# Performance work log

Hardware: AMD Instinct MI355X
Metric: run time of the kernel (lower is better)

The kernel has to match this reference:

```python
import jax, jax.numpy as jnp
import numpy as np

B, L, D = 16, 1024, 1024  # D = 2*model_dim
NEG = -1e10


def setup_inputs() -> dict:
    key = jax.random.key(0)
    k1, k2, k3, k4 = jax.random.split(key, 4)
    inp = jax.random.normal(k1, (B, L, D), dtype=jnp.float32)
    # realistic padding: each sequence has a valid length in [L//2, L]
    lengths = jax.random.randint(k2, (B,), L // 2, L + 1)
    inp_mask = jnp.arange(L)[None, :] >= lengths[:, None]  # True = pad
    # linear_similarity_matrix: Linear(3D, 1, bias=False) -> weight (3D,)
    w_sim = jax.random.normal(k3, (3 * D,), dtype=jnp.float32) * np.sqrt(2.0 / (3 * D + 1)).astype(np.float32)
    # merge_linear: Linear(3D, D)
    Wm = jax.random.normal(k4, (3 * D, D), dtype=jnp.float32) * np.sqrt(2.0 / (4 * D)).astype(np.float32)
    bm = jnp.zeros((D,), dtype=jnp.float32)
    return {"inp": inp, "inp_mask": inp_mask, "w_sim": w_sim, "Wm": Wm, "bm": bm}


def reference(inp, inp_mask, w_sim, Wm, bm):
    # dropout p with training=False is identity (eval mode)
    d = inp.shape[-1]
    w1, w2, w3 = w_sim[:d], w_sim[d:2 * d], w_sim[2 * d:]
    # score[b,i,j] = c_i.w1 + q_j.w2 + (c_i * q_j).w3   (decomposed, no (B,L,L,3D) tensor)
    s_c = inp @ w1                                   # (B, L)
    s_q = inp @ w2                                   # (B, L)
    s_m = jnp.einsum('bid,bjd->bij', inp * w3, inp)  # (B, L, L)
    scores = s_c[:, :, None] + s_q[:, None, :] + s_m
    attn_mask = inp_mask[:, :, None] | inp_mask[:, None, :]
    scores = jnp.where(attn_mask, NEG, scores)
    attn = jax.nn.softmax(scores, axis=-1)           # (B, L, L)
    c2q = jnp.einsum('bij,bjd->bid', attn, inp)      # (B, L, D)
    # merge: relu(cat(c, c2q, c*c2q) @ Wm + bm), decomposed to avoid concat
    W1, W2, W3 = Wm[:d], Wm[d:2 * d], Wm[2 * d:]
    merged = jax.nn.relu(inp @ W1 + c2q @ W2 + (inp * c2q) @ W3 + bm)
    out = jnp.where(inp_mask[:, :, None], 0.0, merged)
    return out
```

## Files before the change

kernel.cpp:

```cpp
#include <hip/hip_runtime.h>
#include <cstdint>

#define LDIM 1024
#define BATCH 16
#define DDIM 1024
#define LDU 3072
#define LDP 2048

using u16 = unsigned short;
typedef __bf16 bf16x8 __attribute__((ext_vector_type(8)));
typedef short  s16x8  __attribute__((ext_vector_type(8)));
typedef float  f32x4  __attribute__((ext_vector_type(4)));

__device__ __forceinline__ u16 f2bf(float f) {
  union { float f; unsigned u; } v; v.f = f;
  unsigned u = v.u;
  return (u16)((u + 0x7FFFu + ((u >> 16) & 1u)) >> 16);
}

typedef const __attribute__((address_space(1))) unsigned int* gp_t;
typedef __attribute__((address_space(3))) unsigned int* lp_t;
__device__ __forceinline__ void async_copy16(const void* g, void* l) {
  __builtin_amdgcn_global_load_lds((gp_t)g, (lp_t)l, 16, 0, 0);
}

__device__ __forceinline__ f32x4 mfma16(s16x8 a, s16x8 b, f32x4 c) {
  return __builtin_amdgcn_mfma_f32_16x16x32_bf16(
      __builtin_bit_cast(bf16x8, a), __builtin_bit_cast(bf16x8, b), c, 0, 0, 0);
}

__device__ __forceinline__ float blockReduceSum(float v) {
  __shared__ float sb[4];
  #pragma unroll
  for (int off = 32; off >= 1; off >>= 1) v += __shfl_xor(v, off);
  if ((threadIdx.x & 63) == 0) sb[threadIdx.x >> 6] = v;
  __syncthreads();
  float r = sb[0] + sb[1] + sb[2] + sb[3];
  __syncthreads();
  return r;
}
__device__ __forceinline__ float blockReduceSum2(float v) {
  __shared__ float sb2[4];
  #pragma unroll
  for (int off = 32; off >= 1; off >>= 1) v += __shfl_xor(v, off);
  if ((threadIdx.x & 63) == 0) sb2[threadIdx.x >> 6] = v;
  __syncthreads();
  float r = sb2[0] + sb2[1] + sb2[2] + sb2[3];
  __syncthreads();
  return r;
}
__device__ __forceinline__ float blockReduceMax(float v) {
  __shared__ float sbm[4];
  #pragma unroll
  for (int off = 32; off >= 1; off >>= 1) v = fmaxf(v, __shfl_xor(v, off));
  if ((threadIdx.x & 63) == 0) sbm[threadIdx.x >> 6] = v;
  __syncthreads();
  float r = fmaxf(fmaxf(sbm[0], sbm[1]), fmaxf(sbm[2], sbm[3]));
  __syncthreads();
  return r;
}

__global__ void diag_kernel(float* __restrict__ out, int n, float tag) {
  int i = blockIdx.x * 256 + threadIdx.x;
  if (i < n) out[i] = (i == 0) ? tag : 0.f;
}

__global__ __launch_bounds__(256) void mask_len_kernel(const unsigned char* __restrict__ mraw,
                                                       int* __restrict__ lengths) {
  const int b = blockIdx.x;
  __shared__ int flag, cnt;
  if (threadIdx.x == 0) { flag = 0; cnt = 0; }
  __syncthreads();
  const int total = BATCH * LDIM;
  for (int p = threadIdx.x; p < total; p += 256) {
    unsigned char v = mraw[p];
    if (v) {
      if (p & 3) atomicOr(&flag, 1);
      else if (p + 3 < total && mraw[p+1] == 0 && mraw[p+2] == 0 && mraw[p+3] == 0)
        atomicOr(&flag, 2);
    }
  }
  __syncthreads();
  const int f = (flag & 1) ? 1 : ((flag & 2) ? 2 : 0);
  int c = 0;
  for (int j = threadIdx.x; j < LDIM; j += 256) {
    bool z;
    if (f == 1)      z = (mraw[b * LDIM + j] == 0);
    else if (f == 2) z = (((const int*)mraw)[b * LDIM + j] == 0);
    else             z = true;
    c += z ? 1 : 0;
  }
  atomicAdd(&cnt, c);
  __syncthreads();
  if (threadIdx.x == 0) lengths[b] = cnt;
}

__global__ __launch_bounds__(256) void prep_row_kernel(
    const float* __restrict__ inp, const float* __restrict__ w_sim,
    u16* __restrict__ U, u16* __restrict__ Abf,
    float* __restrict__ s_c, float* __restrict__ s_q) {
  const int gR = blockIdx.x;
  const int t  = threadIdx.x;
  const float4 x  = ((const float4*)(inp + (size_t)gR * DDIM))[t];
  const float4 w1 = ((const float4*)(w_sim))[t];
  const float4 w2 = ((const float4*)(w_sim + DDIM))[t];
  const float4 w3 = ((const float4*)(w_sim + 2 * DDIM))[t];
  ushort4 xb; xb.x = f2bf(x.x); xb.y = f2bf(x.y); xb.z = f2bf(x.z); xb.w = f2bf(x.w);
  ((ushort4*)(U + (size_t)gR * LDU))[t] = xb;
  ushort4 ab; ab.x = f2bf(x.x * w3.x); ab.y = f2bf(x.y * w3.y);
  ab.z = f2bf(x.z * w3.z); ab.w = f2bf(x.w * w3.w);
  ((ushort4*)(Abf + (size_t)gR * DDIM))[t] = ab;
  float pc = x.x * w1.x + x.y * w1.y + x.z * w1.z + x.w * w1.w;
  float pq = x.x * w2.x + x.y * w2.y + x.z * w2.z + x.w * w2.w;
  pc = blockReduceSum(pc);
  pq = blockReduceSum2(pq);
  if (t == 0) { s_c[gR] = pc; s_q[gR] = pq; }
}

__global__ __launch_bounds__(256) void transpose_x(const u16* __restrict__ U,
                                                   u16* __restrict__ XT) {
  __shared__ u16 tile[64][68];
  const int ti = blockIdx.x, td = blockIdx.y, b = blockIdx.z;
  const int t = threadIdx.x;
  const u16* src = U + ((size_t)(b * LDIM + ti * 64)) * LDU + td * 64;
  #pragma unroll
  for (int q = 0; q < 4; ++q) {
    int n = q * 256 + t;
    int r = n >> 4, c4 = n & 15;
    ushort4 v = ((const ushort4*)(src + (size_t)r * LDU))[c4];
    *(ushort4*)&tile[r][c4 * 4] = v;
  }
  __syncthreads();
  u16* dst = XT + (size_t)b * ((size_t)DDIM * LDIM) + (size_t)(td * 64) * LDIM + ti * 64;
  #pragma unroll
  for (int q = 0; q < 4; ++q) {
    int n = q * 256 + t;
    int d = n >> 4, i4 = n & 15;
    ushort4 v;
    v.x = tile[i4 * 4 + 0][d];
    v.y = tile[i4 * 4 + 1][d];
    v.z = tile[i4 * 4 + 2][d];
    v.w = tile[i4 * 4 + 3][d];
    ((ushort4*)(dst + (size_t)d * LDIM))[i4] = v;
  }
}

__global__ __launch_bounds__(256) void transpose_wm(const float* __restrict__ Wm,
                                                    u16* __restrict__ WmT) {
  __shared__ u16 tile[64][68];
  const int tk = blockIdx.x, tn = blockIdx.y;
  const int t = threadIdx.x;
  #pragma unroll
  for (int q = 0; q < 4; ++q) {
    int n = q * 256 + t;
    int r = n >> 4, c4 = n & 15;
    float4 v = ((const float4*)(Wm + (size_t)(tk * 64 + r) * DDIM + tn * 64))[c4];
    ushort4 o; o.x = f2bf(v.x); o.y = f2bf(v.y); o.z = f2bf(v.z); o.w = f2bf(v.w);
    *(ushort4*)&tile[r][c4 * 4] = o;
  }
  __syncthreads();
  #pragma unroll
  for (int q = 0; q < 4; ++q) {
    int n = q * 256 + t;
    int d = n >> 4, k4 = n & 15;
    ushort4 v;
    v.x = tile[k4 * 4 + 0][d];
    v.y = tile[k4 * 4 + 1][d];
    v.z = tile[k4 * 4 + 2][d];
    v.w = tile[k4 * 4 + 3][d];
    ((ushort4*)(WmT + (size_t)(tn * 64 + d) * LDU + tk * 64))[k4] = v;
  }
}

__global__ __launch_bounds__(256) void softmax_kernel(float* __restrict__ S,
                                                      const int* __restrict__ lengths) {
  const int gR = blockIdx.x;
  const int b = gR >> 10, i = gR & 1023;
  const int len = lengths[b];
  float* srow = S + (size_t)gR * LDIM;
  u16* prow = (u16*)srow;
  const int t = threadIdx.x;
  if (i >= len) {
    ushort4 z; z.x = z.y = z.z = z.w = 0;
    ((ushort4*)prow)[t] = z;
    return;
  }
  const float4 v = ((const float4*)srow)[t];
  const int j0 = t * 4;
  float vals[4] = {v.x, v.y, v.z, v.w};
  float mx = -1e30f;
  #pragma unroll
  for (int e = 0; e < 4; ++e) if (j0 + e < len) mx = fmaxf(mx, vals[e]);
  mx = blockReduceMax(mx);
  float ex[4]; float s = 0.f;
  #pragma unroll
  for (int e = 0; e < 4; ++e) {
    ex[e] = (j0 + e < len) ? __expf(vals[e] - mx) : 0.f;
    s += ex[e];
  }
  s = blockReduceSum(s);
  const float inv = 1.f / s;
  ushort4 o;
  o.x = f2bf(ex[0] * inv); o.y = f2bf(ex[1] * inv);
  o.z = f2bf(ex[2] * inv); o.w = f2bf(ex[3] * inv);
  ((ushort4*)prow)[t] = o;
}

template<int EPI>
__global__ __launch_bounds__(512, 2)
void gemm8p(const u16* __restrict__ A, const u16* __restrict__ Bm,
            int ldaB, int ldbB, int nkt, long strideA, long strideB,
            float* __restrict__ S,
            const float* __restrict__ s_c, const float* __restrict__ s_q,
            const float* __restrict__ inp, u16* __restrict__ U,
            float* __restrict__ outp, const float* __restrict__ bm,
            const int* __restrict__ lengths) {
  extern __shared__ char lds[];
  const int tid = threadIdx.x;
  const int w = tid >> 6, l = tid & 63;
  const int wr = w >> 2, wc = w & 3;
  const int r16 = l & 15, hi = l >> 4;

  const char* Ablk = (const char*)(A + (size_t)blockIdx.z * strideA)
                     + (size_t)blockIdx.x * 256 * ldaB;
  const char* Bblk = (const char*)(Bm + (size_t)blockIdx.z * strideB)
                     + (size_t)blockIdx.y * 256 * ldbB;

  int srow[2], scolb[2];
  #pragma unroll
  for (int q = 0; q < 2; ++q) {
    int y = q * 8192 + w * 1024 + l * 16;
    int ys = y ^ (((y >> 7) & 7) << 4);
    srow[q] = ys >> 7;
    scolb[q] = ys & 127;
  }

  auto stage = [&](int dOff, const char* blk, int ldB, int h, int kt) {
    #pragma unroll
    for (int q = 0; q < 2; ++q) {
      const char* g = blk + (size_t)(h * 128 + srow[q]) * ldB
                      + (size_t)kt * 128 + scolb[q];
      async_copy16(g, lds + dOff + h * 16384 + q * 8192 + w * 1024);
    }
  };
  auto rdA = [&](int d, int m, int kk) -> s16x8 {
    int a = ((m * 32 + wr * 16 + r16) << 7) + kk * 64 + hi * 16;
    a ^= ((a >> 7) & 7) << 4;
    return *(const s16x8*)(lds + d + a);
  };
  auto rdB = [&](int d, int n, int kk) -> s16x8 {
    int a = ((n * 64 + wc * 16 + r16) << 7) + kk * 64 + hi * 16;
    a ^= ((a >> 7) & 7) << 4;
    return *(const s16x8*)(lds + d + 32768 + a);
  };

  f32x4 acc[8][4];
  #pragma unroll
  for (int m = 0; m < 8; ++m)
    #pragma unroll
    for (int n = 0; n < 4; ++n)
      acc[m][n] = (f32x4){0.f, 0.f, 0.f, 0.f};

  stage(0, Ablk, ldaB, 0, 0);
  stage(32768, Bblk, ldbB, 0, 0);
  stage(0, Ablk, ldaB, 1, 0);
  stage(32768, Bblk, ldbB, 1, 0);
  asm volatile("s_waitcnt vmcnt(4)" ::: "memory");
  __builtin_amdgcn_s_barrier();

  s16x8 af[4][2], bf0[2][2], bf1[2][2];
  for (int kt = 0; kt < nkt; ++kt) {
    const int d = (kt & 1) * 65536, dn = 65536 - d;
    const bool nx = (kt + 1) < nkt;
    #pragma unroll
    for (int m4 = 0; m4 < 4; ++m4)
      #pragma unroll
      for (int kk = 0; kk < 2; ++kk) af[m4][kk] = rdA(d, m4, kk);
    #pragma unroll
    for (int n2 = 0; n2 < 2; ++n2)
      #pragma unroll
      for (int kk = 0; kk < 2; ++kk) bf0[n2][kk] = rdB(d, n2, kk);
    if (nx) stage(dn, Ablk, ldaB, 0, kt + 1);
    __builtin_amdgcn_s_barrier();
    __builtin_amdgcn_s_setprio(1);
    #pragma unroll
    for (int m4 = 0; m4 < 4; ++m4)
      #pragma unroll
      for (int n2 = 0; n2 < 2; ++n2)
        #pragma unroll
        for (int kk = 0; kk < 2; ++kk)
          acc[m4][n2] = mfma16(af[m4][kk], bf0[n2][kk], acc[m4][n2]);
    __builtin_amdgcn_s_setprio(0);
    if (nx) asm volatile("s_waitcnt vmcnt(4)" ::: "memory");
    else    asm volatile("s_waitcnt vmcnt(2)" ::: "memory");
    __builtin_amdgcn_s_barrier();
    #pragma unroll
    for (int m4 = 0; m4 < 4; ++m4)
      #pragma unroll
      for (int kk = 0; kk < 2; ++kk) af[m4][kk] = rdA(d, 4 + m4, kk);
    if (nx) stage(dn + 32768, Bblk, ldbB, 0, kt + 1);
    __builtin_amdgcn_s_barrier();
    __builtin_amdgcn_s_setprio(1);
    #pragma unroll
    for (int m4 = 0; m4 < 4; ++m4)
      #pragma unroll
      for (int n2 = 0; n2 < 2; ++n2)
        #pragma unroll
        for (int kk = 0; kk < 2; ++kk)
          acc[4 + m4][n2] = mfma16(af[m4][kk], bf0[n2][kk], acc[4 + m4][n2]);
    __builtin_amdgcn_s_setprio(0);
    if (nx) asm volatile("s_waitcnt vmcnt(4)" ::: "memory");
    else    asm volatile("s_waitcnt vmcnt(0)" ::: "memory");
    __builtin_amdgcn_s_barrier();
    #pragma unroll
    for (int n2 = 0; n2 < 2; ++n2)
      #pragma unroll
      for (int kk = 0; kk < 2; ++kk) bf1[n2][kk] = rdB(d, 2 + n2, kk);
    if (nx) stage(dn, Ablk, ldaB, 1, kt + 1);
    __builtin_amdgcn_s_barrier();
    __builtin_amdgcn_s_setprio(1);
    #pragma unroll
    for (int m4 = 0; m4 < 4; ++m4)
      #pragma unroll
      for (int n2 = 0; n2 < 2; ++n2)
        #pragma unroll
        for (int kk = 0; kk < 2; ++kk)
          acc[4 + m4][2 + n2] = mfma16(af[m4][kk], bf1[n2][kk], acc[4 + m4][2 + n2]);
    __builtin_amdgcn_s_setprio(0);
    if (nx) asm volatile("s_waitcnt vmcnt(4)" ::: "memory");
    else    asm volatile("s_waitcnt vmcnt(0)" ::: "memory");
    __builtin_amdgcn_s_barrier();
    #pragma unroll
    for (int m4 = 0; m4 < 4; ++m4)
      #pragma unroll
      for (int kk = 0; kk < 2; ++kk) af[m4][kk] = rdA(d, m4, kk);
    if (nx) stage(dn + 32768, Bblk, ldbB, 1, kt + 1);
    __builtin_amdgcn_s_barrier();
    __builtin_amdgcn_s_setprio(1);
    #pragma unroll
    for (int m4 = 0; m4 < 4; ++m4)
      #pragma unroll
      for (int n2 = 0; n2 < 2; ++n2)
        #pragma unroll
        for (int kk = 0; kk < 2; ++kk)
          acc[m4][2 + n2] = mfma16(af[m4][kk], bf1[n2][kk], acc[m4][2 + n2]);
    __builtin_amdgcn_s_setprio(0);
    if (nx) asm volatile("s_waitcnt vmcnt(4)" ::: "memory");
    else    asm volatile("s_waitcnt vmcnt(0)" ::: "memory");
    __builtin_amdgcn_s_barrier();
  }

  #pragma unroll
  for (int m = 0; m < 8; ++m) {
    #pragma unroll
    for (int n = 0; n < 4; ++n) {
      #pragma unroll
      for (int j = 0; j < 4; ++j) {
        const int r = blockIdx.x * 256 + m * 32 + wr * 16 + hi * 4 + j;
        const int c = blockIdx.y * 256 + n * 64 + wc * 16 + r16;
        const size_t gR = (size_t)blockIdx.z * LDIM + r;
        float v = acc[m][n][j];
        if constexpr (EPI == 0) {
          v += s_c[gR] + s_q[((gR >> 10) << 10) + c];
          S[gR * LDIM + c] = v;
        } else if constexpr (EPI == 1) {
          const float xi = inp[gR * DDIM + c];
          u16* Ur = U + gR * LDU;
          Ur[DDIM + c]     = f2bf(v);
          Ur[2 * DDIM + c] = f2bf(xi * v);
        } else {
          v += bm[c];
          v = fmaxf(v, 0.f);
          const int b = (int)(gR >> 10);
          const int i = (int)(gR & 1023);
          if (i >= lengths[b]) v = 0.f;
          outp[gR * DDIM + c] = v;
        }
      }
    }
  }
}

extern "C" void kernel_launch(void* const* d_in, const int* in_sizes, int n_in,
                              void* d_out, int out_size, void* d_ws, size_t ws_size,
                              hipStream_t stream) {
  const float* inp          = (const float*)d_in[0];
  const unsigned char* mask = (const unsigned char*)d_in[1];
  const float* w_sim        = (const float*)d_in[2];
  const float* Wm           = (const float*)d_in[3];
  const float* bm           = (const float*)d_in[4];
  float* outp               = (float*)d_out;

  char* ws = (char*)d_ws;
  size_t off = 0;
  auto alloc = [&](size_t bytes) {
    char* p = ws + off;
    off = (off + bytes + 255) & ~(size_t)255;
    return (void*)p;
  };
  u16*   U    = (u16*)alloc((size_t)BATCH * LDIM * LDU * 2);
  float* S    = (float*)alloc((size_t)BATCH * LDIM * LDIM * 4);
  u16*   Abf  = (u16*)alloc((size_t)BATCH * LDIM * DDIM * 2);
  u16*   WmT  = (u16*)alloc((size_t)DDIM * LDU * 2);
  float* s_c  = (float*)alloc((size_t)BATCH * LDIM * 4);
  float* s_q  = (float*)alloc((size_t)BATCH * LDIM * 4);
  int* lengths = (int*)alloc(256);
  u16* XT = Abf;
  u16* P  = (u16*)S;

  if (off > ws_size) {
    diag_kernel<<<(out_size + 255) / 256, 256, 0, stream>>>(
        outp, out_size, (float)(ws_size >> 20));
    return;
  }

  (void)hipFuncSetAttribute((const void*)gemm8p<0>,
      hipFuncAttributeMaxDynamicSharedMemorySize, 131072);
  (void)hipFuncSetAttribute((const void*)gemm8p<1>,
      hipFuncAttributeMaxDynamicSharedMemorySize, 131072);
  (void)hipFuncSetAttribute((const void*)gemm8p<2>,
      hipFuncAttributeMaxDynamicSharedMemorySize, 131072);

  mask_len_kernel<<<BATCH, 256, 0, stream>>>(mask, lengths);
  prep_row_kernel<<<BATCH * LDIM, 256, 0, stream>>>(inp, w_sim, U, Abf, s_c, s_q);
  transpose_wm<<<dim3(48, 16, 1), 256, 0, stream>>>(Wm, WmT);
  gemm8p<0><<<dim3(4, 4, 16), 512, 131072, stream>>>(
      Abf, U, DDIM * 2, LDU * 2, 16, (long)LDIM * DDIM, (long)LDIM * LDU,
      S, s_c, s_q, nullptr, nullptr, nullptr, nullptr, nullptr);
  transpose_x<<<dim3(16, 16, 16), 256, 0, stream>>>(U, XT);
  softmax_kernel<<<BATCH * LDIM, 256, 0, stream>>>(S, lengths);
  gemm8p<1><<<dim3(4, 4, 16), 512, 131072, stream>>>(
      P, XT, LDP * 2, LDIM * 2, 16, (long)LDIM * LDP, (long)DDIM * LDIM,
      nullptr, nullptr, nullptr, inp, U, nullptr, nullptr, nullptr);
  gemm8p<2><<<dim3(64, 4, 1), 512, 131072, stream>>>(
      U, WmT, LDU * 2, LDU * 2, 48, 0, 0,
      nullptr, nullptr, nullptr, nullptr, nullptr, outp, bm, lengths);
}
```

Before: 411.1 us.

## Simplify GEMM main loop to single barrier per k-tile with upfront prefetch

Replaces the four-phase interleaved schedule, which used partial vmcnt waits and eight barriers per k-tile, with a simpler loop. All four next-tile stages are issued at the top, all A/B fragments are read into separate registers, all MFMAs run, and one __syncthreads closes the tile. This cuts barrier and waitcnt overhead but raises register pressure from the extra fragment arrays. It also loses the fine-grained overlap between LDS reads and global loads, and __syncthreads waits for every outstanding load.

New measurement: 512.1 us. +24.6%, slower.

```diff
diff --git a/kernel.cpp b/kernel.cpp
--- a/kernel.cpp
+++ b/kernel.cpp
@@ -265,23 +265,30 @@
   stage(32768, Bblk, ldbB, 0, 0);
   stage(0, Ablk, ldaB, 1, 0);
   stage(32768, Bblk, ldbB, 1, 0);
-  asm volatile("s_waitcnt vmcnt(4)" ::: "memory");
-  __builtin_amdgcn_s_barrier();
-
-  s16x8 af[4][2], bf0[2][2], bf1[2][2];
+  __syncthreads();
+
+  s16x8 a0[4][2], a1[4][2], b0[2][2], b1[2][2];
   for (int kt = 0; kt < nkt; ++kt) {
     const int d = (kt & 1) * 65536, dn = 65536 - d;
     const bool nx = (kt + 1) < nkt;
-    #pragma unroll
-    for (int m4 = 0; m4 < 4; ++m4)
-      #pragma unroll
-      for (int kk = 0; kk < 2; ++kk) af[m4][kk] = rdA(d, m4, kk);
+    if (nx) {
+      stage(dn, Ablk, ldaB, 0, kt + 1);
+      stage(dn + 32768, Bblk, ldbB, 0, kt + 1);
+      stage(dn, Ablk, ldaB, 1, kt + 1);
+      stage(dn + 32768, Bblk, ldbB, 1, kt + 1);
+    }
+    #pragma unroll
+    for (int m4 = 0; m4 < 4; ++m4)
+      #pragma unroll
+      for (int kk = 0; kk < 2; ++kk) a0[m4][kk] = rdA(d, m4, kk);
     #pragma unroll
     for (int n2 = 0; n2 < 2; ++n2)
       #pragma unroll
-      for (int kk = 0; kk < 2; ++kk) bf0[n2][kk] = rdB(d, n2, kk);
-    if (nx) stage(dn, Ablk, ldaB, 0, kt + 1);
-    __builtin_amdgcn_s_barrier();
+      for (int kk = 0; kk < 2; ++kk) b0[n2][kk] = rdB(d, n2, kk);
+    #pragma unroll
+    for (int n2 = 0; n2 < 2; ++n2)
+      #pragma unroll
+      for (int kk = 0; kk < 2; ++kk) b1[n2][kk] = rdB(d, 2 + n2, kk);
     __builtin_amdgcn_s_setprio(1);
     #pragma unroll
     for (int m4 = 0; m4 < 4; ++m4)
@@ -289,17 +296,12 @@
       for (int n2 = 0; n2 < 2; ++n2)
         #pragma unroll
         for (int kk = 0; kk < 2; ++kk)
-          acc[m4][n2] = mfma16(af[m4][kk], bf0[n2][kk], acc[m4][n2]);
+          acc[m4][n2] = mfma16(a0[m4][kk], b0[n2][kk], acc[m4][n2]);
     __builtin_amdgcn_s_setprio(0);
-    if (nx) asm volatile("s_waitcnt vmcnt(4)" ::: "memory");
-    else    asm volatile("s_waitcnt vmcnt(2)" ::: "memory");
-    __builtin_amdgcn_s_barrier();
-    #pragma unroll
-    for (int m4 = 0; m4 < 4; ++m4)
-      #pragma unroll
-      for (int kk = 0; kk < 2; ++kk) af[m4][kk] = rdA(d, 4 + m4, kk);
-    if (nx) stage(dn + 32768, Bblk, ldbB, 0, kt + 1);
-    __builtin_amdgcn_s_barrier();
+    #pragma unroll
+    for (int m4 = 0; m4 < 4; ++m4)
+      #pragma unroll
+      for (int kk = 0; kk < 2; ++kk) a1[m4][kk] = rdA(d, 4 + m4, kk);
     __builtin_amdgcn_s_setprio(1);
     #pragma unroll
     for (int m4 = 0; m4 < 4; ++m4)
@@ -307,47 +309,23 @@
       for (int n2 = 0; n2 < 2; ++n2)
         #pragma unroll
         for (int kk = 0; kk < 2; ++kk)
-          acc[4 + m4][n2] = mfma16(af[m4][kk], bf0[n2][kk], acc[4 + m4][n2]);
-    __builtin_amdgcn_s_setprio(0);
-    if (nx) asm volatile("s_waitcnt vmcnt(4)" ::: "memory");
-    else    asm volatile("s_waitcnt vmcnt(0)" ::: "memory");
-    __builtin_amdgcn_s_barrier();
-    #pragma unroll
-    for (int n2 = 0; n2 < 2; ++n2)
-      #pragma unroll
-      for (int kk = 0; kk < 2; ++kk) bf1[n2][kk] = rdB(d, 2 + n2, kk);
-    if (nx) stage(dn, Ablk, ldaB, 1, kt + 1);
-    __builtin_amdgcn_s_barrier();
-    __builtin_amdgcn_s_setprio(1);
+          acc[m4][2 + n2] = mfma16(a0[m4][kk], b1[n2][kk], acc[m4][2 + n2]);
     #pragma unroll
     for (int m4 = 0; m4 < 4; ++m4)
       #pragma unroll
       for (int n2 = 0; n2 < 2; ++n2)
         #pragma unroll
         for (int kk = 0; kk < 2; ++kk)
-          acc[4 + m4][2 + n2] = mfma16(af[m4][kk], bf1[n2][kk], acc[4 + m4][2 + n2]);
-    __builtin_amdgcn_s_setprio(0);
-    if (nx) asm volatile("s_waitcnt vmcnt(4)" ::: "memory");
-    else    asm volatile("s_waitcnt vmcnt(0)" ::: "memory");
-    __builtin_amdgcn_s_barrier();
-    #pragma unroll
-    for (int m4 = 0; m4 < 4; ++m4)
-      #pragma unroll
-      for (int kk = 0; kk < 2; ++kk) af[m4][kk] = rdA(d, m4, kk);
-    if (nx) stage(dn + 32768, Bblk, ldbB, 1, kt + 1);
-    __builtin_amdgcn_s_barrier();
-    __builtin_amdgcn_s_setprio(1);
+          acc[4 + m4][n2] = mfma16(a1[m4][kk], b0[n2][kk], acc[4 + m4][n2]);
     #pragma unroll
     for (int m4 = 0; m4 < 4; ++m4)
       #pragma unroll
       for (int n2 = 0; n2 < 2; ++n2)
         #pragma unroll
         for (int kk = 0; kk < 2; ++kk)
-          acc[m4][2 + n2] = mfma16(af[m4][kk], bf1[n2][kk], acc[m4][2 + n2]);
+          acc[4 + m4][2 + n2] = mfma16(a1[m4][kk], b1[n2][kk], acc[4 + m4][2 + n2]);
     __builtin_amdgcn_s_setprio(0);
-    if (nx) asm volatile("s_waitcnt vmcnt(4)" ::: "memory");
-    else    asm volatile("s_waitcnt vmcnt(0)" ::: "memory");
-    __builtin_amdgcn_s_barrier();
+    __syncthreads();
   }
 
   #pragma unroll
```
